# Performance work log

Measured on AMD Instinct MI355X. Metric: run time of the kernel, lower is better.

Reference implementation:

```python
import jax, jax.numpy as jnp
import numpy as np

# Fixed hyperparameters from init_kwargs
KH, KW = 3, 3
GRID_SIZE = 5
SPLINE_ORDER = 3
GRID_RANGE = (-1.0, 1.0)


def _make_grid():
    # grid buffer: arange(-k, grid_size + k + 1) * h + grid_range[0], shape (G + 2k + 1,) = (12,)
    h = (GRID_RANGE[1] - GRID_RANGE[0]) / GRID_SIZE
    return (jnp.arange(-SPLINE_ORDER, GRID_SIZE + SPLINE_ORDER + 1, dtype=jnp.float32) * h
            + GRID_RANGE[0])


def _unfold(x):
    # torch.nn.Unfold with kernel (3,3), stride 1, pad 0, dilation 1.
    # Returns (N, C*KH*KW) with channel-major ordering (c, i, j), matching torch.
    B, C, H, W = x.shape
    Ho, Wo = H - KH + 1, W - KW + 1
    cols = [x[:, :, i:i + Ho, j:j + Wo] for i in range(KH) for j in range(KW)]
    p = jnp.stack(cols, axis=2)                    # (B, C, KH*KW, Ho, Wo)
    p = p.reshape(B, C * KH * KW, Ho * Wo)         # (B, in_features, L)
    p = p.transpose(0, 2, 1).reshape(-1, C * KH * KW)  # (B*L, in_features)
    return p, Ho, Wo


def _b_splines(x, grid):
    # x: (N, in_features); grid: (G + 2k + 1,) uniform, shared across features.
    # Returns (N, in_features, G + k) B-spline basis via Cox-de Boor recursion.
    x = x[..., None]  # (N, in, 1)
    bases = ((x >= grid[:-1]) & (x < grid[1:])).astype(x.dtype)  # (N, in, G+2k)
    for k in range(1, SPLINE_ORDER + 1):
        left = (x - grid[: -(k + 1)]) / (grid[k:-1] - grid[: -(k + 1)])
        right = (grid[k + 1:] - x) / (grid[k + 1:] - grid[1:-k])
        bases = left * bases[..., :-1] + right * bases[..., 1:]
    return bases  # (N, in, G + k)


def setup_inputs() -> dict:
    key = jax.random.key(0)
    k1, k2, k3, k4 = jax.random.split(key, 4)
    in_features = 32 * KH * KW  # 288
    out_features = 64
    n_coef = GRID_SIZE + SPLINE_ORDER  # 8
    x = jax.random.normal(k1, (16, 32, 64, 64), dtype=jnp.float32)
    base_weight = jax.random.normal(k2, (out_features, in_features), dtype=jnp.float32) * (1.0 / np.sqrt(in_features))
    spline_weight = jax.random.normal(k3, (out_features, in_features, n_coef), dtype=jnp.float32) * 0.1
    spline_scaler = jax.random.normal(k4, (out_features, in_features), dtype=jnp.float32) * (1.0 / np.sqrt(in_features))
    return {"x": x, "base_weight": base_weight, "spline_weight": spline_weight,
            "spline_scaler": spline_scaler}


def reference(x, base_weight, spline_weight, spline_scaler):
    B = x.shape[0]
    out_features = base_weight.shape[0]
    grid = _make_grid()

    patches, Ho, Wo = _unfold(x)                              # (N, in_features)
    N, in_features = patches.shape

    # KANLinear forward
    base_out = jnp.matmul(jax.nn.relu(patches), base_weight.T)  # (N, out)
    bases = _b_splines(patches, grid)                           # (N, in, G+k)
    scaled_w = spline_weight * spline_scaler[..., None]         # (out, in, G+k)
    spline_out = jnp.matmul(bases.reshape(N, -1), scaled_w.reshape(out_features, -1).T)
    out = base_out + spline_out                                 # (N, out)

    out = out.reshape(B, Ho, Wo, out_features).transpose(0, 3, 1, 2)  # (B, C_out, Ho, Wo)
    return out
```

## Files before the change

### kernel.cpp

```cpp
#include <hip/hip_runtime.h>
#include <stdint.h>

typedef _Float16 half8  __attribute__((ext_vector_type(8)));
typedef float    f32x4  __attribute__((ext_vector_type(4)));
typedef uint32_t u32x4  __attribute__((ext_vector_type(4)));

#define FIN  288
#define NOUT 64
#define LPB  3844
#define KSPL 72
#define SC   200
#define LDSN (31*SC + 2*64 + 64 + 8)


__global__ void prep_bfrag(const float* __restrict__ bw,
                           const float* __restrict__ sw,
                           const float* __restrict__ sc,
                           half8* __restrict__ bfrag) {
  int t = blockIdx.x * 256 + threadIdx.x;
  half8 v;
  int dst;
  if (t < NOUT * FIN) {
    int o = t / FIN;
    int f = t - o * FIN;
    float scale = sc[t];
    const float* p = sw + t * 8;
#pragma unroll
    for (int c = 0; c < 8; ++c) v[c] = (_Float16)(p[c] * scale);
    int ch = f / 9;
    int r  = f - ch * 9;
    int ii = r / 3;
    int jj = r - ii * 3;
    int g  = ch >> 2, q = ch & 3;
    int kt = ii * 24 + jj * 8 + g;
    dst = (kt * 4 + (o >> 4)) * 64 + q * 16 + (o & 15);
  } else {
    int t2 = t - NOUT * FIN;
    int lane = t2 & 63;
    int nf = (t2 >> 6) & 3;
    int ktb = t2 >> 8;
    int o = nf * 16 + (lane & 15);
    int f0 = ktb * 32 + (lane >> 4) * 8;
    const float* p = bw + o * FIN + f0;
#pragma unroll
    for (int c = 0; c < 8; ++c) v[c] = (_Float16)p[c];
    dst = ((KSPL + ktb) * 4 + nf) * 64 + lane;
  }
  bfrag[dst] = v;
}

__device__ inline half8 bspline8(float xv) {
  float u = fmaf(xv, 2.5f, 5.5f);
  float fi = floorf(u);
  int i = (int)fi;
  float t = u - fi, s = 1.0f - t;
  float t2 = t * t, t3 = t2 * t;
  float s2 = s * s, s3 = s2 * s;
  float w3 = t3 * 0.16666667f;
  float w0 = s3 * 0.16666667f;
  float w1 = fmaf(0.5f, t3, -t2) + 0.66666667f;
  float w2 = fmaf(0.5f, s3, -s2) + 0.66666667f;
  uint32_t u01 = __builtin_bit_cast(uint32_t, __builtin_amdgcn_cvt_pkrtz(w0, w1));
  uint32_t u23 = __builtin_bit_cast(uint32_t, __builtin_amdgcn_cvt_pkrtz(w2, w3));
  uint64_t V = (uint64_t)u01 | ((uint64_t)u23 << 32);
  uint32_t vl = (uint32_t)(V << 16);
  u32x4 fr;
#pragma unroll
  for (int q = 0; q < 4; ++q) {
    int d = i - 2 * q;
    uint32_t rr = (uint32_t)(V >> ((48 - 16 * d) & 63));
    fr[q] = ((uint32_t)d <= 3u) ? rr : ((d == 4) ? vl : 0u);
  }
  return __builtin_bit_cast(half8, fr);
}

__global__ __launch_bounds__(256, 4) void kan_main(
    const float* __restrict__ x,
    const half8* __restrict__ bfrag,
    float* __restrict__ out) {
  __shared__ float lx[LDSN];

  const int tid = threadIdx.x;
  const int bid = blockIdx.x;
  const int b  = bid / 62;
  const int ho = bid - b * 62;

  const float* xb = x + b * 131072 + ho * 64;
#pragma unroll
  for (int r = 0; r < 6; ++r) {
    int gid = r * 256 + tid;
    int row = gid >> 4;
    int c   = (row * 683) >> 11;
    int ii  = row - c * 3;
    int colv = (gid & 15) * 4;
    const float4 v = *(const float4*)(xb + c * 4096 + ii * 64 + colv);
    *(float4*)(&lx[c * SC + ii * 64 + colv]) = v;
  }
  __syncthreads();

  const int lane = tid & 63;
  const int wv   = tid >> 6;
  const int quad = lane >> 4;
  const int m16  = lane & 15;
  const int wo   = wv * 16 + m16;

  f32x4 acc[4];
#pragma unroll
  for (int nf = 0; nf < 4; ++nf) acc[nf] = (f32x4){0.f, 0.f, 0.f, 0.f};

  int kt = 0;
#pragma unroll
  for (int ii = 0; ii < 3; ++ii) {
#pragma unroll
    for (int jj = 0; jj < 3; ++jj) {
      const float* lbase = lx + quad * SC + ii * 64 + wo + jj;
#pragma unroll
      for (int g = 0; g < 8; ++g) {
        float xv = lbase[g * (4 * SC)];
        half8 af = bspline8(xv);
#pragma unroll
        for (int nf = 0; nf < 4; ++nf) {
          half8 bf = bfrag[(kt * 4 + nf) * 64 + lane];
          acc[nf] = __builtin_amdgcn_mfma_f32_16x16x32_f16(af, bf, acc[nf], 0, 0, 0);
        }
        ++kt;
      }
    }
  }

#pragma unroll
  for (int kb = 0; kb < 9; ++kb) {
    int f0 = kb * 32 + quad * 8;
    half8 a;
#pragma unroll
    for (int j = 0; j < 8; ++j) {
      int f = f0 + j;
      int c = (f * 57) >> 9;
      int r = f - c * 9;
      int i2 = (r * 11) >> 5;
      int j2 = r - i2 * 3;
      a[j] = (_Float16)fmaxf(lx[c * SC + i2 * 64 + wo + j2], 0.0f);
    }
#pragma unroll
    for (int nf = 0; nf < 4; ++nf) {
      half8 bf = bfrag[((KSPL + kb) * 4 + nf) * 64 + lane];
      acc[nf] = __builtin_amdgcn_mfma_f32_16x16x32_f16(a, bf, acc[nf], 0, 0, 0);
    }
  }

  float* ob = out + b * (NOUT * LPB) + ho * 62;
#pragma unroll
  for (int rg = 0; rg < 4; ++rg) {
    int wo2 = wv * 16 + quad * 4 + rg;
    if (wo2 < 62) {
#pragma unroll
      for (int nf = 0; nf < 4; ++nf) {
        int o = nf * 16 + m16;
        ob[o * LPB + wo2] = acc[nf][rg];
      }
    }
  }
}

extern "C" void kernel_launch(void* const* d_in, const int* in_sizes, int n_in,
                              void* d_out, int out_size, void* d_ws, size_t ws_size,
                              hipStream_t stream) {
  const float* x  = (const float*)d_in[0];
  const float* bw = (const float*)d_in[1];
  const float* sw = (const float*)d_in[2];
  const float* sc = (const float*)d_in[3];
  float* out = (float*)d_out;
  half8* bfrag = (half8*)d_ws;

  prep_bfrag<<<81, 256, 0, stream>>>(bw, sw, sc, bfrag);
  kan_main<<<16 * 62, 256, 0, stream>>>(x, bfrag, out);
}
```

Measured before the change: 121.3 us.

## Precompute B-spline basis per input pixel once, then gather in main GEMM kernel

Adds a pre-pass that evaluates the 8 cubic B-spline weights once per input element and stores them as fp16 half8 in workspace. A new main kernel gathers these vectors directly from global memory instead of recomputing the basis nine times per element (once per kernel tap) from LDS. In exchange it writes and reads a 32 MB intermediate buffer, drops the LDS staging, and uses uncoalesced-ish per-pixel gathers. It falls back to the old kernel if the workspace is too small.

```diff
diff --git a/kernel.cpp b/kernel.cpp
--- a/kernel.cpp
+++ b/kernel.cpp
@@ -5,13 +5,15 @@
 typedef float    f32x4  __attribute__((ext_vector_type(4)));
 typedef uint32_t u32x4  __attribute__((ext_vector_type(4)));
 
+#define NPIX 61504
+#define LPB  3844
 #define FIN  288
 #define NOUT 64
-#define LPB  3844
 #define KSPL 72
-#define SC   200
-#define LDSN (31*SC + 2*64 + 64 + 8)
-
+#define NXPIX 2097152
+#define BFRAG_BYTES 332800
+#define BSP_BYTES   (NXPIX * 16)
+#define WS_NEED     ((size_t)BFRAG_BYTES + (size_t)BSP_BYTES)
 
 __global__ void prep_bfrag(const float* __restrict__ bw,
                            const float* __restrict__ sw,
@@ -74,17 +76,99 @@
   return __builtin_bit_cast(half8, fr);
 }
 
-__global__ __launch_bounds__(256, 4) void kan_main(
+__global__ void precompute_basis(const float* __restrict__ x,
+                                 half8* __restrict__ bsp) {
+  int i = blockIdx.x * 256 + threadIdx.x;
+  bsp[i] = bspline8(x[i]);
+}
+
+__global__ __launch_bounds__(256, 4) void kan_main2(
+    const float* __restrict__ x,
+    const half8* __restrict__ bsp,
+    const half8* __restrict__ bfrag,
+    float* __restrict__ out) {
+  const int lane = threadIdx.x & 63;
+  const int wv   = threadIdx.x >> 6;
+  const int quad = lane >> 4;
+  const int m16  = lane & 15;
+
+  const int px = blockIdx.x * 64 + wv * 16 + m16;
+  const int b  = px / LPB;
+  const int l  = px - b * LPB;
+  const int ho = l / 62;
+  const int wo = l - ho * 62;
+  const int xbase = b * 131072 + ho * 64 + wo;
+
+  f32x4 acc[4];
+#pragma unroll
+  for (int nf = 0; nf < 4; ++nf) acc[nf] = (f32x4){0.f, 0.f, 0.f, 0.f};
+
+  const half8* abase = bsp + xbase + quad * 4096;
+
+  int kt = 0;
+#pragma unroll
+  for (int ii = 0; ii < 3; ++ii) {
+#pragma unroll
+    for (int jj = 0; jj < 3; ++jj) {
+      const half8* ap = abase + ii * 64 + jj;
+#pragma unroll
+      for (int g = 0; g < 8; ++g) {
+        half8 af = ap[g * 16384];
+#pragma unroll
+        for (int nf = 0; nf < 4; ++nf) {
+          half8 bf = bfrag[(kt * 4 + nf) * 64 + lane];
+          acc[nf] = __builtin_amdgcn_mfma_f32_16x16x32_f16(af, bf, acc[nf], 0, 0, 0);
+        }
+        ++kt;
+      }
+    }
+  }
+
+#pragma unroll
+  for (int kb = 0; kb < 9; ++kb) {
+    int f0 = kb * 32 + quad * 8;
+    half8 a;
+#pragma unroll
+    for (int j = 0; j < 8; ++j) {
+      int f = f0 + j;
+      int c = (f * 57) >> 9;
+      int r = f - c * 9;
+      int i2 = (r * 11) >> 5;
+      int j2 = r - i2 * 3;
+      a[j] = (_Float16)fmaxf(x[xbase + c * 4096 + i2 * 64 + j2], 0.0f);
+    }
+#pragma unroll
+    for (int nf = 0; nf < 4; ++nf) {
+      half8 bf = bfrag[((KSPL + kb) * 4 + nf) * 64 + lane];
+      acc[nf] = __builtin_amdgcn_mfma_f32_16x16x32_f16(a, bf, acc[nf], 0, 0, 0);
+    }
+  }
+
+#pragma unroll
+  for (int rg = 0; rg < 4; ++rg) {
+    int p2 = blockIdx.x * 64 + wv * 16 + quad * 4 + rg;
+    int b2 = p2 / LPB;
+    int l2 = p2 - b2 * LPB;
+    float* ob = out + b2 * (NOUT * LPB) + l2;
+#pragma unroll
+    for (int nf = 0; nf < 4; ++nf) {
+      int o = nf * 16 + m16;
+      ob[o * LPB] = acc[nf][rg];
+    }
+  }
+}
+
+#define SC   200
+#define LDSN (31*SC + 2*64 + 64 + 8)
+__global__ __launch_bounds__(256, 4) void kan_main_fb(
     const float* __restrict__ x,
     const half8* __restrict__ bfrag,
     float* __restrict__ out) {
   __shared__ float lx[LDSN];
-
   const int tid = threadIdx.x;
   const int bid = blockIdx.x;
   const int b  = bid / 62;
   const int ho = bid - b * 62;
-
   const float* xb = x + b * 131072 + ho * 64;
 #pragma unroll
   for (int r = 0; r < 6; ++r) {
@@ -97,17 +181,14 @@
     *(float4*)(&lx[c * SC + ii * 64 + colv]) = v;
   }
   __syncthreads();
-
   const int lane = tid & 63;
   const int wv   = tid >> 6;
   const int quad = lane >> 4;
   const int m16  = lane & 15;
   const int wo   = wv * 16 + m16;
-
   f32x4 acc[4];
 #pragma unroll
   for (int nf = 0; nf < 4; ++nf) acc[nf] = (f32x4){0.f, 0.f, 0.f, 0.f};
-
   int kt = 0;
 #pragma unroll
   for (int ii = 0; ii < 3; ++ii) {
@@ -127,7 +208,6 @@
       }
     }
   }
-
 #pragma unroll
   for (int kb = 0; kb < 9; ++kb) {
     int f0 = kb * 32 + quad * 8;
@@ -147,7 +227,6 @@
       acc[nf] = __builtin_amdgcn_mfma_f32_16x16x32_f16(a, bf, acc[nf], 0, 0, 0);
     }
   }
-
   float* ob = out + b * (NOUT * LPB) + ho * 62;
 #pragma unroll
   for (int rg = 0; rg < 4; ++rg) {
@@ -171,7 +250,13 @@
   const float* sc = (const float*)d_in[3];
   float* out = (float*)d_out;
   half8* bfrag = (half8*)d_ws;
+  half8* bsp   = (half8*)((char*)d_ws + BFRAG_BYTES);
 
   prep_bfrag<<<81, 256, 0, stream>>>(bw, sw, sc, bfrag);
-  kan_main<<<16 * 62, 256, 0, stream>>>(x, bfrag, out);
-}
+  if (ws_size >= WS_NEED) {
+    precompute_basis<<<NXPIX / 256, 256, 0, stream>>>(x, bsp);
+    kan_main2<<<NPIX / 64, 256, 0, stream>>>(x, bsp, bfrag, out);
+  } else {
+    kan_main_fb<<<16 * 62, 256, 0, stream>>>(x, bfrag, out);
+  }
+}
```

Result: slower. 139.3 us (+14.9%).

## Precompute B-spline fragments per input element and flatten the pixel tiling

Applied to the files above, without the earlier changes.

A prep kernel now evaluates the cubic B-spline fp16 fragment once for every input element and writes it to workspace. The main kernel gathers those fragments from global memory instead of recomputing them nine times per element from LDS. The LDS staging is removed, and blocks now cover flat 64-pixel tiles with a remapped block order. The trade is less per-element arithmetic for about 32MB of extra workspace write and read traffic, plus gather loads that may miss in cache.

```diff
diff --git a/kernel.cpp b/kernel.cpp
--- a/kernel.cpp
+++ b/kernel.cpp
@@ -5,19 +5,52 @@
 typedef float    f32x4  __attribute__((ext_vector_type(4)));
 typedef uint32_t u32x4  __attribute__((ext_vector_type(4)));
 
+#define NPIX 61504
+#define LPB  3844
 #define FIN  288
 #define NOUT 64
-#define LPB  3844
 #define KSPL 72
-#define SC   200
-#define LDSN (31*SC + 2*64 + 64 + 8)
+#define NXPIX 2097152
+#define BFRAG_BYTES 332800
 
+__device__ inline half8 bspline8(float xv) {
+  float u = fmaf(xv, 2.5f, 5.5f);
+  float fi = floorf(u);
+  int i = (int)fi;
+  float t = u - fi, s = 1.0f - t;
+  float t2 = t * t, t3 = t2 * t;
+  float s2 = s * s, s3 = s2 * s;
+  float w3 = t3 * 0.16666667f;
+  float w0 = s3 * 0.16666667f;
+  float w1 = fmaf(0.5f, t3, -t2) + 0.66666667f;
+  float w2 = fmaf(0.5f, s3, -s2) + 0.66666667f;
+  uint32_t u01 = __builtin_bit_cast(uint32_t, __builtin_amdgcn_cvt_pkrtz(w0, w1));
+  uint32_t u23 = __builtin_bit_cast(uint32_t, __builtin_amdgcn_cvt_pkrtz(w2, w3));
+  uint64_t V = (uint64_t)u01 | ((uint64_t)u23 << 32);
+  uint32_t vl = (uint32_t)(V << 16);
+  u32x4 fr;
+#pragma unroll
+  for (int q = 0; q < 4; ++q) {
+    int d = i - 2 * q;
+    uint32_t rr = (uint32_t)(V >> ((48 - 16 * d) & 63));
+    fr[q] = ((uint32_t)d <= 3u) ? rr : ((d == 4) ? vl : 0u);
+  }
+  return __builtin_bit_cast(half8, fr);
+}
 
-__global__ void prep_bfrag(const float* __restrict__ bw,
-                           const float* __restrict__ sw,
-                           const float* __restrict__ sc,
-                           half8* __restrict__ bfrag) {
-  int t = blockIdx.x * 256 + threadIdx.x;
+__global__ void prep_all(const float* __restrict__ x,
+                         const float* __restrict__ bw,
+                         const float* __restrict__ sw,
+                         const float* __restrict__ sc,
+                         half8* __restrict__ bsp,
+                         half8* __restrict__ bfrag) {
+  int bid = blockIdx.x;
+  if (bid < 8192) {
+    int i = bid * 256 + threadIdx.x;
+    bsp[i] = bspline8(x[i]);
+    return;
+  }
+  int t = (bid - 8192) * 256 + threadIdx.x;
   half8 v;
   int dst;
   if (t < NOUT * FIN) {
@@ -49,75 +82,41 @@
   bfrag[dst] = v;
 }
 
-__device__ inline half8 bspline8(float xv) {
-  float u = fmaf(xv, 2.5f, 5.5f);
-  float fi = floorf(u);
-  int i = (int)fi;
-  float t = u - fi, s = 1.0f - t;
-  float t2 = t * t, t3 = t2 * t;
-  float s2 = s * s, s3 = s2 * s;
-  float w3 = t3 * 0.16666667f;
-  float w0 = s3 * 0.16666667f;
-  float w1 = fmaf(0.5f, t3, -t2) + 0.66666667f;
-  float w2 = fmaf(0.5f, s3, -s2) + 0.66666667f;
-  uint32_t u01 = __builtin_bit_cast(uint32_t, __builtin_amdgcn_cvt_pkrtz(w0, w1));
-  uint32_t u23 = __builtin_bit_cast(uint32_t, __builtin_amdgcn_cvt_pkrtz(w2, w3));
-  uint64_t V = (uint64_t)u01 | ((uint64_t)u23 << 32);
-  uint32_t vl = (uint32_t)(V << 16);
-  u32x4 fr;
-#pragma unroll
-  for (int q = 0; q < 4; ++q) {
-    int d = i - 2 * q;
-    uint32_t rr = (uint32_t)(V >> ((48 - 16 * d) & 63));
-    fr[q] = ((uint32_t)d <= 3u) ? rr : ((d == 4) ? vl : 0u);
-  }
-  return __builtin_bit_cast(half8, fr);
-}
-
-__global__ __launch_bounds__(256, 4) void kan_main(
+__global__ __launch_bounds__(256, 4) void kan_main2(
     const float* __restrict__ x,
+    const half8* __restrict__ bsp,
     const half8* __restrict__ bfrag,
     float* __restrict__ out) {
-  __shared__ float lx[LDSN];
-
-  const int tid = threadIdx.x;
-  const int bid = blockIdx.x;
-  const int b  = bid / 62;
-  const int ho = bid - b * 62;
-
-  const float* xb = x + b * 131072 + ho * 64;
-#pragma unroll
-  for (int r = 0; r < 6; ++r) {
-    int gid = r * 256 + tid;
-    int row = gid >> 4;
-    int c   = (row * 683) >> 11;
-    int ii  = row - c * 3;
-    int colv = (gid & 15) * 4;
-    const float4 v = *(const float4*)(xb + c * 4096 + ii * 64 + colv);
-    *(float4*)(&lx[c * SC + ii * 64 + colv]) = v;
-  }
-  __syncthreads();
-
-  const int lane = tid & 63;
-  const int wv   = tid >> 6;
+  const int lane = threadIdx.x & 63;
+  const int wv   = threadIdx.x >> 6;
   const int quad = lane >> 4;
   const int m16  = lane & 15;
-  const int wo   = wv * 16 + m16;
+
+  const int bid  = blockIdx.x;
+  const int tile = (bid < 960) ? ((bid & 7) * 120 + (bid >> 3)) : 960;
+
+  const int px = tile * 64 + wv * 16 + m16;
+  const int b  = px / LPB;
+  const int l  = px - b * LPB;
+  const int ho = l / 62;
+  const int wo = l - ho * 62;
+  const int xbase = b * 131072 + ho * 64 + wo;
 
   f32x4 acc[4];
 #pragma unroll
   for (int nf = 0; nf < 4; ++nf) acc[nf] = (f32x4){0.f, 0.f, 0.f, 0.f};
+
+  const half8* abase = bsp + xbase + quad * 4096;
 
   int kt = 0;
 #pragma unroll
   for (int ii = 0; ii < 3; ++ii) {
 #pragma unroll
     for (int jj = 0; jj < 3; ++jj) {
-      const float* lbase = lx + quad * SC + ii * 64 + wo + jj;
+      const half8* ap = abase + ii * 64 + jj;
 #pragma unroll
       for (int g = 0; g < 8; ++g) {
-        float xv = lbase[g * (4 * SC)];
-        half8 af = bspline8(xv);
+        half8 af = ap[g * 16384];
 #pragma unroll
         for (int nf = 0; nf < 4; ++nf) {
           half8 bf = bfrag[(kt * 4 + nf) * 64 + lane];
@@ -139,7 +138,7 @@
       int r = f - c * 9;
       int i2 = (r * 11) >> 5;
       int j2 = r - i2 * 3;
-      a[j] = (_Float16)fmaxf(lx[c * SC + i2 * 64 + wo + j2], 0.0f);
+      a[j] = (_Float16)fmaxf(x[xbase + c * 4096 + i2 * 64 + j2], 0.0f);
     }
 #pragma unroll
     for (int nf = 0; nf < 4; ++nf) {
@@ -148,16 +147,16 @@
     }
   }
 
-  float* ob = out + b * (NOUT * LPB) + ho * 62;
 #pragma unroll
   for (int rg = 0; rg < 4; ++rg) {
-    int wo2 = wv * 16 + quad * 4 + rg;
-    if (wo2 < 62) {
+    int p2 = tile * 64 + wv * 16 + quad * 4 + rg;
+    int b2 = p2 / LPB;
+    int l2 = p2 - b2 * LPB;
+    float* ob = out + b2 * (NOUT * LPB) + l2;
 #pragma unroll
-      for (int nf = 0; nf < 4; ++nf) {
-        int o = nf * 16 + m16;
-        ob[o * LPB + wo2] = acc[nf][rg];
-      }
+    for (int nf = 0; nf < 4; ++nf) {
+      int o = nf * 16 + m16;
+      ob[o * LPB] = acc[nf][rg];
     }
   }
 }
@@ -171,7 +170,8 @@
   const float* sc = (const float*)d_in[3];
   float* out = (float*)d_out;
   half8* bfrag = (half8*)d_ws;
+  half8* bsp   = (half8*)((char*)d_ws + BFRAG_BYTES);
 
-  prep_bfrag<<<81, 256, 0, stream>>>(bw, sw, sc, bfrag);
-  kan_main<<<16 * 62, 256, 0, stream>>>(x, bfrag, out);
+  prep_all<<<8192 + 81, 256, 0, stream>>>(x, bw, sw, sc, bsp, bfrag);
+  kan_main2<<<NPIX / 64, 256, 0, stream>>>(x, bsp, bfrag, out);
 }
```

Measured after the change: 139.6 us. +15.1%, slower.
